# Kernel tuning notes

Hardware: AMD Instinct MI355X
Metric: run time of the kernel (lower is better)

The kernel has to match this reference:

```python
import jax, jax.numpy as jnp
import numpy as np

N = 20000       # nodes
E = 320000      # edges (before self-loops)
F_IN = 128
HID = 128
HEADS = 4
OUT_DIM = 2
B = 64          # graphs in batch
SLOPE = 0.2     # GATv2 leaky_relu negative slope (PyG default)


def _glorot(key, shape):
    fan_in, fan_out = shape[0], shape[1]
    limit = np.sqrt(6.0 / (fan_in + fan_out)).astype(np.float32)
    return jax.random.uniform(key, shape, jnp.float32, -limit, limit)


def setup_inputs() -> dict:
    key = jax.random.key(0)
    ks = jax.random.split(key, 24)
    inp = {
        'x': jax.random.normal(ks[0], (N, F_IN), jnp.float32),
        'edge_src': jax.random.randint(ks[1], (E,), 0, N),
        'edge_dst': jax.random.randint(ks[2], (E,), 0, N),
        'batch': jnp.sort(jax.random.randint(ks[3], (N,), 0, B)),
        # layer 1: in=F_IN, out=HEADS*HID, concat
        'Wl1': _glorot(ks[4], (F_IN, HEADS * HID)),
        'Wr1': _glorot(ks[5], (F_IN, HEADS * HID)),
        'bl1': jnp.zeros((HEADS * HID,), jnp.float32),
        'br1': jnp.zeros((HEADS * HID,), jnp.float32),
        'att1': _glorot(ks[6], (HEADS, HID)),
        'bias1': jnp.zeros((HEADS * HID,), jnp.float32),
        # layer 2: in=HEADS*HID, out=HEADS*HID, concat
        'Wl2': _glorot(ks[7], (HEADS * HID, HEADS * HID)),
        'Wr2': _glorot(ks[8], (HEADS * HID, HEADS * HID)),
        'bl2': jnp.zeros((HEADS * HID,), jnp.float32),
        'br2': jnp.zeros((HEADS * HID,), jnp.float32),
        'att2': _glorot(ks[9], (HEADS, HID)),
        'bias2': jnp.zeros((HEADS * HID,), jnp.float32),
        # layer 3: in=HEADS*HID, heads=1, concat=False -> out=HID
        'Wl3': _glorot(ks[10], (HEADS * HID, HID)),
        'Wr3': _glorot(ks[11], (HEADS * HID, HID)),
        'bl3': jnp.zeros((HID,), jnp.float32),
        'br3': jnp.zeros((HID,), jnp.float32),
        'att3': _glorot(ks[12], (1, HID)),
        'bias3': jnp.zeros((HID,), jnp.float32),
        # output MLP
        'W_mlp1': _glorot(ks[13], (HID, HID)),
        'b_mlp1': jnp.zeros((HID,), jnp.float32),
        'W_mlp2': _glorot(ks[14], (HID, OUT_DIM)),
        'b_mlp2': jnp.zeros((OUT_DIM,), jnp.float32),
    }
    return inp


def gatv2_layer(x, src, dst, Wl, Wr, bl, br, att, bias, concat):
    """PyG GATv2Conv (eval mode): alpha_ij = softmax_j over N(i) of a^T LeakyReLU(xl_j + xr_i)."""
    H, C = att.shape
    n = x.shape[0]
    xl = (x @ Wl + bl).reshape(n, H, C)   # source transform
    e = jax.nn.leaky_relu(xl[src] + (x @ Wr + br).reshape(n, H, C)[dst], SLOPE)  # [E,H,C]
    logits = jnp.einsum('ehc,hc->eh', e, att)                                    # [E,H]
    # segment softmax over destination node
    m = jax.ops.segment_max(logits, dst, num_segments=n)
    alpha = jnp.exp(logits - m[dst])
    denom = jax.ops.segment_sum(alpha, dst, num_segments=n)
    alpha = alpha / denom[dst]
    out = jax.ops.segment_sum(xl[src] * alpha[..., None], dst, num_segments=n)   # [N,H,C]
    out = out.reshape(n, H * C) if concat else out.mean(axis=1)
    return out + bias


def reference(x, edge_src, edge_dst, batch,
              Wl1, Wr1, bl1, br1, att1, bias1,
              Wl2, Wr2, bl2, br2, att2, bias2,
              Wl3, Wr3, bl3, br3, att3, bias3,
              W_mlp1, b_mlp1, W_mlp2, b_mlp2):
    n = x.shape[0]
    loop = jnp.arange(n, dtype=edge_src.dtype)
    src = jnp.concatenate([edge_src, loop])   # PyG add_self_loops=True
    dst = jnp.concatenate([edge_dst, loop])

    h = jax.nn.elu(gatv2_layer(x, src, dst, Wl1, Wr1, bl1, br1, att1, bias1, True))
    h = jax.nn.elu(gatv2_layer(h, src, dst, Wl2, Wr2, bl2, br2, att2, bias2, True))
    h = jax.nn.elu(gatv2_layer(h, src, dst, Wl3, Wr3, bl3, br3, att3, bias3, False))

    # global_mean_pool over graph ids
    counts = jnp.maximum(jax.ops.segment_sum(jnp.ones((n,), h.dtype), batch, num_segments=B), 1.0)
    pooled = jax.ops.segment_sum(h, batch, num_segments=B) / counts[:, None]

    hidden = jax.nn.relu(pooled @ W_mlp1 + b_mlp1)
    return hidden @ W_mlp2 + b_mlp2
```

## Files before the change

kernel.cpp:

```cpp
#include <hip/hip_runtime.h>
#include <math.h>


typedef __attribute__((ext_vector_type(4))) float f32x4;
typedef __attribute__((ext_vector_type(8))) _Float16 f16x8;
typedef __attribute__((ext_vector_type(4))) _Float16 f16x4;
typedef __attribute__((ext_vector_type(2))) _Float16 f16x2;

__device__ __forceinline__ float elu1(float x) {
    return (x > 0.f) ? x : (__expf(x) - 1.f);
}
__device__ __forceinline__ float leaky02(float x) {
    return (x >= 0.f) ? x : 0.2f * x;
}
__device__ __forceinline__ f16x2 pk_leaky(f16x2 s) {
    const f16x2 slope = {(_Float16)0.2f, (_Float16)0.2f};
    return __builtin_elementwise_max(s, s * slope);
}

__global__ void zero32_kernel(int* __restrict__ p, int n) {
    int i = blockIdx.x * 256 + threadIdx.x;
    if (i < n) p[i] = 0;
}

__global__ void count_kernel(const int* __restrict__ dst, int* __restrict__ cnt,
                             int E, int N) {
    int e = blockIdx.x * 256 + threadIdx.x;
    if (e < E + N) {
        int d = (e < E) ? dst[e] : (e - E);
        atomicAdd(&cnt[d], 1);
    }
}

__global__ __launch_bounds__(1024) void scan_kernel(const int* __restrict__ cnt,
                                                    int* __restrict__ rowstart,
                                                    int* __restrict__ cursor,
                                                    int N, int total) {
    __shared__ int part[1024];
    int t = threadIdx.x;
    int ch = (N + 1023) >> 10;
    int base = t * ch;
    int loc[32];
    int s = 0;
    for (int i = 0; i < ch && i < 32; ++i) {
        int idx = base + i;
        int v = (idx < N) ? cnt[idx] : 0;
        loc[i] = s;
        s += v;
    }
    part[t] = s;
    __syncthreads();
    for (int off = 1; off < 1024; off <<= 1) {
        int v = (t >= off) ? part[t - off] : 0;
        __syncthreads();
        part[t] += v;
        __syncthreads();
    }
    int excl = (t == 0) ? 0 : part[t - 1];
    for (int i = 0; i < ch && i < 32; ++i) {
        int idx = base + i;
        if (idx < N) {
            int v = excl + loc[i];
            rowstart[idx] = v;
            cursor[idx]   = v;
        }
    }
    if (t == 0) rowstart[N] = total;
}

__global__ void scatter_kernel(const int* __restrict__ src, const int* __restrict__ dst,
                               int* __restrict__ cursor, int* __restrict__ csr_src,
                               int E, int N) {
    int e = blockIdx.x * 256 + threadIdx.x;
    if (e < E + N) {
        int d, s;
        if (e < E) { d = dst[e]; s = src[e]; }
        else       { d = e - E; s = e - E; }
        int pos = atomicAdd(&cursor[d], 1);
        csr_src[pos] = s;
    }
}

__global__ void boundary_kernel(const int* __restrict__ batch,
                                int* __restrict__ gstart, int N, int B) {
    int n = blockIdx.x * 256 + threadIdx.x;
    if (n > N) return;
    int cur  = (n < N) ? batch[n] : B;
    int prev = (n == 0) ? -1 : batch[n - 1];
    for (int g = prev + 1; g <= cur; ++g) gstart[g] = n;
}

__global__ void convA_kernel(const float* __restrict__ X, _Float16* __restrict__ A,
                             int n_valid, int n_total) {
    int i = (blockIdx.x * 256 + threadIdx.x) * 4;
    if (i >= n_total) return;
    float4 v = (i < n_valid) ? *(const float4*)(X + i) : make_float4(0.f, 0.f, 0.f, 0.f);
    f16x4 h;
    h.x = (_Float16)v.x; h.y = (_Float16)v.y;
    h.z = (_Float16)v.z; h.w = (_Float16)v.w;
    *(f16x4*)(A + i) = h;
}

__global__ __launch_bounds__(256) void convWT_kernel(
    const float* __restrict__ Wl, const float* __restrict__ Wr,
    _Float16* __restrict__ Bth, _Float16* __restrict__ Btl, int K, int Nh) {
    __shared__ float tile[32][33];
    int kb = blockIdx.x * 32;
    int nb = blockIdx.y * 32;
    int tx = threadIdx.x;
    int ty = threadIdx.y;
#pragma unroll
    for (int j = 0; j < 4; ++j) {
        int kk = kb + ty + j * 8;
        int nn = nb + tx;
        float v = (nn < Nh) ? Wl[(size_t)kk * Nh + nn]
                            : Wr[(size_t)kk * Nh + (nn - Nh)];
        tile[ty + j * 8][tx] = v;
    }
    __syncthreads();
#pragma unroll
    for (int j = 0; j < 4; ++j) {
        int nn = nb + ty + j * 8;
        int kk = kb + tx;
        float v = tile[tx][ty + j * 8];
        _Float16 h = (_Float16)v;
        Bth[(size_t)nn * K + kk] = h;
        Btl[(size_t)nn * K + kk] = (_Float16)(v - (float)h);
    }
}

#define SCW 132
__global__ __launch_bounds__(256, 1) void gemm_f16_kernel(
    const _Float16* __restrict__ A,
    const _Float16* __restrict__ Bh, const _Float16* __restrict__ Bl,
    const float* __restrict__ biasL, const float* __restrict__ biasR, int Nh_,
    _Float16* __restrict__ P, _Float16* __restrict__ Q, int K, int NT) {
    __shared__ __align__(16) char smem[49152];
    _Float16* sA[2]  = { (_Float16*)(smem),         (_Float16*)(smem + 24576) };
    _Float16* sBh[2] = { (_Float16*)(smem + 8192),  (_Float16*)(smem + 32768) };
    _Float16* sBl[2] = { (_Float16*)(smem + 16384), (_Float16*)(smem + 40960) };
    float*    sC     = (float*)(smem);

    const int tid  = threadIdx.x;
    const int lane = tid & 63;
    const int wv   = tid >> 6;
    const int wm   = wv & 1;
    const int wn   = wv >> 1;
    const int fm   = lane & 15;
    const int q    = lane >> 4;

    const int bi = blockIdx.x;
    const int kx = bi & 7;
    const int tt = bi >> 3;
    const int m0 = ((tt / NT) * 8 + kx) * 128;
    const int n0 = (tt % NT) * 128;

    const int r0  = lane >> 2;
    const int kco = (lane & 3) << 3;

    f32x4 acc[4][4];
#pragma unroll
    for (int i = 0; i < 4; ++i)
#pragma unroll
        for (int j = 0; j < 4; ++j) {
            acc[i][j].x = 0.f; acc[i][j].y = 0.f;
            acc[i][j].z = 0.f; acc[i][j].w = 0.f;
        }

    for (int k0 = 0; k0 < K; k0 += 64) {
        __syncthreads();
#pragma unroll
        for (int s = 0; s < 2; ++s) {
            int ks = k0 + s * 32;
#pragma unroll
            for (int j = 0; j < 2; ++j) {
                int wc  = wv * 2 + j;
                int row = wc * 16 + r0;
                size_t ga = (size_t)(m0 + row) * K + ks + kco;
                size_t gb = (size_t)(n0 + row) * K + ks + kco;
                int lofs = wc * 512;
                __builtin_amdgcn_global_load_lds(
                    (const __attribute__((address_space(1))) void*)(A + ga),
                    (__attribute__((address_space(3))) void*)(sA[s] + lofs), 16, 0, 0);
                __builtin_amdgcn_global_load_lds(
                    (const __attribute__((address_space(1))) void*)(Bh + gb),
                    (__attribute__((address_space(3))) void*)(sBh[s] + lofs), 16, 0, 0);
                __builtin_amdgcn_global_load_lds(
                    (const __attribute__((address_space(1))) void*)(Bl + gb),
                    (__attribute__((address_space(3))) void*)(sBl[s] + lofs), 16, 0, 0);
            }
        }
        __syncthreads();

#pragma unroll
        for (int s = 0; s < 2; ++s) {
            f16x8 ah[4];
#pragma unroll
            for (int mi = 0; mi < 4; ++mi)
                ah[mi] = *(const f16x8*)&sA[s][(wm * 64 + mi * 16 + fm) * 32 + q * 8];
#pragma unroll
            for (int ni = 0; ni < 4; ++ni) {
                int r = (wn * 64 + ni * 16 + fm) * 32 + q * 8;
                f16x8 bh = *(const f16x8*)&sBh[s][r];
                f16x8 bl = *(const f16x8*)&sBl[s][r];
#pragma unroll
                for (int mi = 0; mi < 4; ++mi) {
                    acc[mi][ni] = __builtin_amdgcn_mfma_f32_16x16x32_f16(ah[mi], bh, acc[mi][ni], 0, 0, 0);
                    acc[mi][ni] = __builtin_amdgcn_mfma_f32_16x16x32_f16(ah[mi], bl, acc[mi][ni], 0, 0, 0);
                }
            }
        }
    }

    float bsv[4];
#pragma unroll
    for (int ni = 0; ni < 4; ++ni) {
        int col = n0 + wn * 64 + ni * 16 + fm;
        bsv[ni] = (col < Nh_) ? biasL[col] : biasR[col - Nh_];
    }

    _Float16* dstbase = (n0 < Nh_) ? P : Q;
    const int col0 = (n0 < Nh_) ? n0 : (n0 - Nh_);

#pragma unroll
    for (int c = 0; c < 2; ++c) {
        __syncthreads();
        if (wm == c) {
#pragma unroll
            for (int mi = 0; mi < 4; ++mi)
#pragma unroll
                for (int ni = 0; ni < 4; ++ni) {
                    int base = (mi * 16 + q * 4) * SCW + wn * 64 + ni * 16 + fm;
                    sC[base]           = acc[mi][ni].x + bsv[ni];
                    sC[base + SCW]     = acc[mi][ni].y + bsv[ni];
                    sC[base + 2 * SCW] = acc[mi][ni].z + bsv[ni];
                    sC[base + 3 * SCW] = acc[mi][ni].w + bsv[ni];
                }
        }
        __syncthreads();
#pragma unroll
        for (int j = 0; j < 8; ++j) {
            int flat = j * 256 + tid;
            int row  = flat >> 5;
            int col  = (flat & 31) * 4;
            f32x4 v = *(const f32x4*)(sC + row * SCW + col);
            f16x4 hv;
            hv.x = (_Float16)v.x; hv.y = (_Float16)v.y;
            hv.z = (_Float16)v.z; hv.w = (_Float16)v.w;
            *(f16x4*)(dstbase + (size_t)(m0 + c * 64 + row) * Nh_ + col0 + col) = hv;
        }
    }
}

__global__ __launch_bounds__(256) void gat_edge4_kernel(
    const _Float16* __restrict__ P, const _Float16* __restrict__ Q,
    const float* __restrict__ att, const float* __restrict__ bias,
    const int* __restrict__ rowstart, const int* __restrict__ srcs,
    _Float16* __restrict__ H, int N) {
    __shared__ float s_m[4][4];
    __shared__ float s_l[4][4];
    __shared__ float s_acc[4][512];

    int n = blockIdx.x;
    int wv = threadIdx.x >> 6;
    int lane = threadIdx.x & 63;
    int c0 = lane * 8;
    int h = lane >> 4;

    f16x8 rv = *(const f16x8*)(Q + (size_t)n * 512 + c0);
    f16x2 r2[4];
#pragma unroll
    for (int k = 0; k < 4; ++k) { r2[k].x = rv[2 * k]; r2[k].y = rv[2 * k + 1]; }
    float tf[8];
#pragma unroll
    for (int j = 0; j < 8; ++j) tf[j] = att[c0 + j];

    float acc[8];
#pragma unroll
    for (int j = 0; j < 8; ++j) acc[j] = 0.f;
    float m_run = -1e30f, l_run = 0.f;

    int beg = rowstart[n], end = rowstart[n + 1];
    int i = beg + wv * 2;
    for (; i + 1 < end; i += 8) {
        int s0 = srcs[i];
        int s1 = srcs[i + 1];
        f16x8 hv0 = *(const f16x8*)(P + (size_t)s0 * 512 + c0);
        f16x8 hv1 = *(const f16x8*)(P + (size_t)s1 * 512 + c0);
        float p0 = 0.f, p1 = 0.f;
#pragma unroll
        for (int k = 0; k < 4; ++k) {
            f16x2 a0; a0.x = hv0[2 * k]; a0.y = hv0[2 * k + 1];
            f16x2 a1; a1.x = hv1[2 * k]; a1.y = hv1[2 * k + 1];
            f16x2 m0v = pk_leaky(a0 + r2[k]);
            f16x2 m1v = pk_leaky(a1 + r2[k]);
            p0 = fmaf((float)m0v.x, tf[2 * k], p0);
            p0 = fmaf((float)m0v.y, tf[2 * k + 1], p0);
            p1 = fmaf((float)m1v.x, tf[2 * k], p1);
            p1 = fmaf((float)m1v.y, tf[2 * k + 1], p1);
        }
        p0 += __shfl_xor(p0, 1, 16);
        p1 += __shfl_xor(p1, 1, 16);
        p0 += __shfl_xor(p0, 2, 16);
        p1 += __shfl_xor(p1, 2, 16);
        p0 += __shfl_xor(p0, 4, 16);
        p1 += __shfl_xor(p1, 4, 16);
        p0 += __shfl_xor(p0, 8, 16);
        p1 += __shfl_xor(p1, 8, 16);
        float m01 = fmaxf(p0, p1);
        float w0 = __expf(p0 - m01);
        float w1 = __expf(p1 - m01);
        float pl = w0 + w1;
        float m_new = fmaxf(m_run, m01);
        float sc = __expf(m_run - m_new);
        float sp = __expf(m01 - m_new);
        l_run = l_run * sc + pl * sp;
        float ws0 = w0 * sp;
        float ws1 = w1 * sp;
#pragma unroll
        for (int j = 0; j < 8; ++j) {
            float a = acc[j] * sc;
            a = fmaf((float)hv0[j], ws0, a);
            acc[j] = fmaf((float)hv1[j], ws1, a);
        }
        m_run = m_new;
    }
    if (i < end) {
        int s = srcs[i];
        f16x8 hv = *(const f16x8*)(P + (size_t)s * 512 + c0);
        float p = 0.f;
#pragma unroll
        for (int k = 0; k < 4; ++k) {
            f16x2 a; a.x = hv[2 * k]; a.y = hv[2 * k + 1];
            f16x2 mv = pk_leaky(a + r2[k]);
            p = fmaf((float)mv.x, tf[2 * k], p);
            p = fmaf((float)mv.y, tf[2 * k + 1], p);
        }
        p += __shfl_xor(p, 1, 16);
        p += __shfl_xor(p, 2, 16);
        p += __shfl_xor(p, 4, 16);
        p += __shfl_xor(p, 8, 16);
        float m_new = fmaxf(m_run, p);
        float sc = __expf(m_run - m_new);
        float al = __expf(p - m_new);
        l_run = l_run * sc + al;
#pragma unroll
        for (int j = 0; j < 8; ++j)
            acc[j] = fmaf((float)hv[j], al, acc[j] * sc);
        m_run = m_new;
    }
    if ((lane & 15) == 0) { s_m[wv][h] = m_run; s_l[wv][h] = l_run; }
    *(float4*)&s_acc[wv][c0]     = make_float4(acc[0], acc[1], acc[2], acc[3]);
    *(float4*)&s_acc[wv][c0 + 4] = make_float4(acc[4], acc[5], acc[6], acc[7]);
    __syncthreads();
    if (wv == 0) {
        float M = fmaxf(fmaxf(s_m[0][h], s_m[1][h]), fmaxf(s_m[2][h], s_m[3][h]));
        float L = 0.f;
        float o[8];
#pragma unroll
        for (int j = 0; j < 8; ++j) o[j] = 0.f;
#pragma unroll
        for (int w = 0; w < 4; ++w) {
            float sc = __expf(s_m[w][h] - M);
            L += s_l[w][h] * sc;
            float4 q0 = *(const float4*)&s_acc[w][c0];
            float4 q1 = *(const float4*)&s_acc[w][c0 + 4];
            o[0] += q0.x * sc; o[1] += q0.y * sc; o[2] += q0.z * sc; o[3] += q0.w * sc;
            o[4] += q1.x * sc; o[5] += q1.y * sc; o[6] += q1.z * sc; o[7] += q1.w * sc;
        }
        float inv = 1.f / L;
        f16x8 oh;
#pragma unroll
        for (int j = 0; j < 8; ++j)
            oh[j] = (_Float16)elu1(o[j] * inv + bias[c0 + j]);
        *(f16x8*)(H + (size_t)n * 512 + c0) = oh;
    }
}

__global__ __launch_bounds__(256) void gat_edge1_kernel(
    const _Float16* __restrict__ P, const _Float16* __restrict__ Q,
    const float* __restrict__ att, const float* __restrict__ bias,
    const int* __restrict__ rowstart, const int* __restrict__ srcs,
    float* __restrict__ out, int N) {
    __shared__ float s_m[4];
    __shared__ float s_l[4];
    __shared__ float s_acc[4][128];

    int n = blockIdx.x;
    int wv = threadIdx.x >> 6;
    int lane = threadIdx.x & 63;
    int c0 = lane * 2;

    f16x2 rv = *(const f16x2*)(Q + (size_t)n * 128 + c0);
    float2 t = *(const float2*)(att + c0);

    float acc0 = 0.f, acc1 = 0.f;
    float m_run = -1e30f, l_run = 0.f;

    int beg = rowstart[n], end = rowstart[n + 1];
    int i = beg + wv * 2;
    for (; i + 1 < end; i += 8) {
        int s0 = srcs[i];
        int s1 = srcs[i + 1];
        f16x2 h0 = *(const f16x2*)(P + (size_t)s0 * 128 + c0);
        f16x2 h1 = *(const f16x2*)(P + (size_t)s1 * 128 + c0);
        f16x2 m0v = pk_leaky(h0 + rv);
        f16x2 m1v = pk_leaky(h1 + rv);
        float p0 = fmaf((float)m0v.x, t.x, (float)m0v.y * t.y);
        float p1 = fmaf((float)m1v.x, t.x, (float)m1v.y * t.y);
        p0 += __shfl_xor(p0, 1, 64);
        p1 += __shfl_xor(p1, 1, 64);
        p0 += __shfl_xor(p0, 2, 64);
        p1 += __shfl_xor(p1, 2, 64);
        p0 += __shfl_xor(p0, 4, 64);
        p1 += __shfl_xor(p1, 4, 64);
        p0 += __shfl_xor(p0, 8, 64);
        p1 += __shfl_xor(p1, 8, 64);
        p0 += __shfl_xor(p0, 16, 64);
        p1 += __shfl_xor(p1, 16, 64);
        p0 += __shfl_xor(p0, 32, 64);
        p1 += __shfl_xor(p1, 32, 64);
        float m01 = fmaxf(p0, p1);
        float w0 = __expf(p0 - m01);
        float w1 = __expf(p1 - m01);
        float pl  = w0 + w1;
        float m_new = fmaxf(m_run, m01);
        float sc = __expf(m_run - m_new);
        float sp = __expf(m01 - m_new);
        float ws0 = w0 * sp;
        float ws1 = w1 * sp;
        l_run = l_run * sc + pl * sp;
        acc0 = fmaf((float)h1.x, ws1, fmaf((float)h0.x, ws0, acc0 * sc));
        acc1 = fmaf((float)h1.y, ws1, fmaf((float)h0.y, ws0, acc1 * sc));
        m_run = m_new;
    }
    if (i < end) {
        int s = srcs[i];
        f16x2 hv = *(const f16x2*)(P + (size_t)s * 128 + c0);
        f16x2 mv = pk_leaky(hv + rv);
        float p = fmaf((float)mv.x, t.x, (float)mv.y * t.y);
        p += __shfl_xor(p, 1, 64);
        p += __shfl_xor(p, 2, 64);
        p += __shfl_xor(p, 4, 64);
        p += __shfl_xor(p, 8, 64);
        p += __shfl_xor(p, 16, 64);
        p += __shfl_xor(p, 32, 64);
        float m_new = fmaxf(m_run, p);
        float sc = __expf(m_run - m_new);
        float al = __expf(p - m_new);
        l_run = l_run * sc + al;
        acc0 = fmaf((float)hv.x, al, acc0 * sc);
        acc1 = fmaf((float)hv.y, al, acc1 * sc);
        m_run = m_new;
    }
    if (lane == 0) { s_m[wv] = m_run; s_l[wv] = l_run; }
    *(float2*)&s_acc[wv][c0] = make_float2(acc0, acc1);
    __syncthreads();
    if (wv == 0) {
        float M = fmaxf(fmaxf(s_m[0], s_m[1]), fmaxf(s_m[2], s_m[3]));
        float L = 0.f, o0 = 0.f, o1 = 0.f;
#pragma unroll
        for (int w = 0; w < 4; ++w) {
            float sc = __expf(s_m[w] - M);
            L += s_l[w] * sc;
            float2 qv = *(const float2*)&s_acc[w][c0];
            o0 += qv.x * sc;
            o1 += qv.y * sc;
        }
        float inv = 1.f / L;
        float2 w2;
        w2.x = elu1(o0 * inv + bias[c0]);
        w2.y = elu1(o1 * inv + bias[c0 + 1]);
        *(float2*)(out + (size_t)n * 128 + c0) = w2;
    }
}

__global__ __launch_bounds__(256) void pool2_kernel(
    const float* __restrict__ h3, const int* __restrict__ gstart,
    float* __restrict__ pooled) {
    __shared__ float red[256];
    int g = blockIdx.x;
    int c = threadIdx.x & 127;
    int h = threadIdx.x >> 7;
    int gs = gstart[g], ge = gstart[g + 1];
    float s = 0.f;
    for (int n = gs + h; n < ge; n += 2) s += h3[(size_t)n * 128 + c];
    red[threadIdx.x] = s;
    __syncthreads();
    if (h == 0) {
        float tot = red[c] + red[c + 128];
        float cnt = fmaxf((float)(ge - gs), 1.f);
        pooled[g * 128 + c] = tot / cnt;
    }
}

__global__ __launch_bounds__(128) void mlp_kernel(
    const float* __restrict__ pooled,
    const float* __restrict__ W1, const float* __restrict__ b1,
    const float* __restrict__ W2, const float* __restrict__ b2,
    float* __restrict__ out) {
    __shared__ float pr[128];
    __shared__ float2 red[128];
    int g = blockIdx.x;
    int t = threadIdx.x;
    pr[t] = pooled[g * 128 + t];
    __syncthreads();
    float h = b1[t];
#pragma unroll 4
    for (int k = 0; k < 128; ++k) h = fmaf(pr[k], W1[k * 128 + t], h);
    h = fmaxf(h, 0.0f);
    red[t] = make_float2(h * W2[t * 2], h * W2[t * 2 + 1]);
    __syncthreads();
    for (int s = 64; s > 0; s >>= 1) {
        if (t < s) {
            red[t].x += red[t + s].x;
            red[t].y += red[t + s].y;
        }
        __syncthreads();
    }
    if (t == 0) {
        out[g * 2]     = red[0].x + b2[0];
        out[g * 2 + 1] = red[0].y + b2[1];
    }
}

extern "C" void kernel_launch(void* const* d_in, const int* in_sizes, int n_in,
                              void* d_out, int out_size, void* d_ws, size_t ws_size,
                              hipStream_t stream) {
    const float* x     = (const float*)d_in[0];
    const int*   esrc  = (const int*)d_in[1];
    const int*   edst  = (const int*)d_in[2];
    const int*   batch = (const int*)d_in[3];
    const float* Wl1   = (const float*)d_in[4];
    const float* Wr1   = (const float*)d_in[5];
    const float* bl1   = (const float*)d_in[6];
    const float* br1   = (const float*)d_in[7];
    const float* att1  = (const float*)d_in[8];
    const float* bias1 = (const float*)d_in[9];
    const float* Wl2   = (const float*)d_in[10];
    const float* Wr2   = (const float*)d_in[11];
    const float* bl2   = (const float*)d_in[12];
    const float* br2   = (const float*)d_in[13];
    const float* att2  = (const float*)d_in[14];
    const float* bias2 = (const float*)d_in[15];
    const float* Wl3   = (const float*)d_in[16];
    const float* Wr3   = (const float*)d_in[17];
    const float* bl3   = (const float*)d_in[18];
    const float* br3   = (const float*)d_in[19];
    const float* att3  = (const float*)d_in[20];
    const float* bias3 = (const float*)d_in[21];
    const float* Wm1   = (const float*)d_in[22];
    const float* bm1   = (const float*)d_in[23];
    const float* Wm2   = (const float*)d_in[24];
    const float* bm2   = (const float*)d_in[25];

    int N  = in_sizes[0] / 128;
    int E  = in_sizes[1];
    int ET = E + N;
    int B  = out_size / 2;
    const int Mp = 160 * 128;

    char* ws = (char*)d_ws;
    size_t off = 0;
    auto alloc = [&](size_t bytes) -> void* {
        void* p = ws + off;
        off += (bytes + 255) & ~(size_t)255;
        return p;
    };
    _Float16* P    = (_Float16*)alloc((size_t)Mp * 512 * 2);
    _Float16* Q    = (_Float16*)alloc((size_t)Mp * 512 * 2);
    _Float16* A1   = (_Float16*)alloc((size_t)Mp * 128 * 2);
    _Float16* Hb   = (_Float16*)alloc((size_t)Mp * 512 * 2);
    _Float16* Wth1 = (_Float16*)alloc((size_t)1024 * 128 * 2);
    _Float16* Wtl1 = (_Float16*)alloc((size_t)1024 * 128 * 2);
    _Float16* Wth2 = (_Float16*)alloc((size_t)1024 * 512 * 2);
    _Float16* Wtl2 = (_Float16*)alloc((size_t)1024 * 512 * 2);
    _Float16* Wth3 = (_Float16*)alloc((size_t)256 * 512 * 2);
    _Float16* Wtl3 = (_Float16*)alloc((size_t)256 * 512 * 2);
    float*    R3   = (float*)alloc((size_t)Mp * 128 * 4);
    int*    cnt      = (int*)alloc((size_t)N * 4);
    int*    rowstart = (int*)alloc((size_t)(N + 1) * 4);
    int*    cursor   = (int*)alloc((size_t)N * 4);
    int*    csr_src  = (int*)alloc((size_t)ET * 4);
    int*    gstart   = (int*)alloc((size_t)(B + 1) * 4);
    float*  pooled   = (float*)alloc((size_t)B * 128 * 4);
    (void)ws_size;

    zero32_kernel<<<(N + 255) / 256, 256, 0, stream>>>(cnt, N);

    count_kernel<<<(ET + 255) / 256, 256, 0, stream>>>(edst, cnt, E, N);
    scan_kernel<<<1, 1024, 0, stream>>>(cnt, rowstart, cursor, N, ET);
    scatter_kernel<<<(ET + 255) / 256, 256, 0, stream>>>(esrc, edst, cursor, csr_src, E, N);
    boundary_kernel<<<(N + 256) / 256, 256, 0, stream>>>(batch, gstart, N, B);

    convWT_kernel<<<dim3(4, 32),  dim3(32, 8), 0, stream>>>(Wl1, Wr1, Wth1, Wtl1, 128, 512);
    convWT_kernel<<<dim3(16, 32), dim3(32, 8), 0, stream>>>(Wl2, Wr2, Wth2, Wtl2, 512, 512);
    convWT_kernel<<<dim3(16, 8),  dim3(32, 8), 0, stream>>>(Wl3, Wr3, Wth3, Wtl3, 512, 128);

    convA_kernel<<<((Mp * 128 / 4) + 255) / 256, 256, 0, stream>>>(x, A1, N * 128, Mp * 128);

    gemm_f16_kernel<<<160 * 8, 256, 0, stream>>>(A1, Wth1, Wtl1, bl1, br1, 512, P, Q, 128, 8);
    gat_edge4_kernel<<<N, 256, 0, stream>>>(P, Q, att1, bias1, rowstart, csr_src, Hb, N);

    gemm_f16_kernel<<<160 * 8, 256, 0, stream>>>(Hb, Wth2, Wtl2, bl2, br2, 512, P, Q, 512, 8);
    gat_edge4_kernel<<<N, 256, 0, stream>>>(P, Q, att2, bias2, rowstart, csr_src, Hb, N);

    gemm_f16_kernel<<<160 * 2, 256, 0, stream>>>(Hb, Wth3, Wtl3, bl3, br3, 128, P, Q, 512, 2);
    gat_edge1_kernel<<<N, 256, 0, stream>>>(P, Q, att3, bias3, rowstart, csr_src, R3, N);

    pool2_kernel<<<B, 256, 0, stream>>>(R3, gstart, pooled);
    mlp_kernel<<<B, 128, 0, stream>>>(pooled, Wm1, bm1, Wm2, bm2, (float*)d_out);
}
```

Baseline: 469.7 us.

## Double-buffer GEMM K-loop to prefetch the next slice during MFMA

```diff
diff --git a/kernel.cpp b/kernel.cpp
--- a/kernel.cpp
+++ b/kernel.cpp
@@ -9,9 +9,6 @@
 
 __device__ __forceinline__ float elu1(float x) {
     return (x > 0.f) ? x : (__expf(x) - 1.f);
-}
-__device__ __forceinline__ float leaky02(float x) {
-    return (x >= 0.f) ? x : 0.2f * x;
 }
 __device__ __forceinline__ f16x2 pk_leaky(f16x2 s) {
     const f16x2 slope = {(_Float16)0.2f, (_Float16)0.2f};
@@ -136,10 +133,7 @@
     const float* __restrict__ biasL, const float* __restrict__ biasR, int Nh_,
     _Float16* __restrict__ P, _Float16* __restrict__ Q, int K, int NT) {
     __shared__ __align__(16) char smem[49152];
-    _Float16* sA[2]  = { (_Float16*)(smem),         (_Float16*)(smem + 24576) };
-    _Float16* sBh[2] = { (_Float16*)(smem + 8192),  (_Float16*)(smem + 32768) };
-    _Float16* sBl[2] = { (_Float16*)(smem + 16384), (_Float16*)(smem + 40960) };
-    float*    sC     = (float*)(smem);
+    float* sC = (float*)(smem);
 
     const int tid  = threadIdx.x;
     const int lane = tid & 63;
@@ -158,6 +152,7 @@
     const int r0  = lane >> 2;
     const int kco = (lane & 3) << 3;
 
+
     f32x4 acc[4][4];
 #pragma unroll
     for (int i = 0; i < 4; ++i)
@@ -167,49 +162,71 @@
             acc[i][j].z = 0.f; acc[i][j].w = 0.f;
         }
 
-    for (int k0 = 0; k0 < K; k0 += 64) {
+    const int nIters = K >> 5;
+    int cur = 0;
+    {
+        char* base = smem;
+#pragma unroll
+        for (int j = 0; j < 2; ++j) {
+            int wc  = wv * 2 + j;
+            int row = wc * 16 + r0;
+            size_t ga = (size_t)(m0 + row) * K + kco;
+            size_t gb = (size_t)(n0 + row) * K + kco;
+            int lofs = wc * 1024;
+            __builtin_amdgcn_global_load_lds(
+                (const __attribute__((address_space(1))) void*)(A + ga),
+                (__attribute__((address_space(3))) void*)(base + lofs), 16, 0, 0);
+            __builtin_amdgcn_global_load_lds(
+                (const __attribute__((address_space(1))) void*)(Bh + gb),
+                (__attribute__((address_space(3))) void*)(base + 8192 + lofs), 16, 0, 0);
+            __builtin_amdgcn_global_load_lds(
+                (const __attribute__((address_space(1))) void*)(Bl + gb),
+                (__attribute__((address_space(3))) void*)(base + 16384 + lofs), 16, 0, 0);
+        }
+    }
+    for (int it = 0; it < nIters; ++it) {
         __syncthreads();
-#pragma unroll
-        for (int s = 0; s < 2; ++s) {
-            int ks = k0 + s * 32;
+        if (it + 1 < nIters) {
+            char* base = smem + (cur ^ 1) * 24576;
+            int ks = (it + 1) << 5;
 #pragma unroll
             for (int j = 0; j < 2; ++j) {
                 int wc  = wv * 2 + j;
                 int row = wc * 16 + r0;
                 size_t ga = (size_t)(m0 + row) * K + ks + kco;
                 size_t gb = (size_t)(n0 + row) * K + ks + kco;
-                int lofs = wc * 512;
+                int lofs = wc * 1024;
                 __builtin_amdgcn_global_load_lds(
                     (const __attribute__((address_space(1))) void*)(A + ga),
-                    (__attribute__((address_space(3))) void*)(sA[s] + lofs), 16, 0, 0);
+                    (__attribute__((address_space(3))) void*)(base + lofs), 16, 0, 0);
                 __builtin_amdgcn_global_load_lds(
                     (const __attribute__((address_space(1))) void*)(Bh + gb),
-                    (__attribute__((address_space(3))) void*)(sBh[s] + lofs), 16, 0, 0);
+                    (__attribute__((address_space(3))) void*)(base + 8192 + lofs), 16, 0, 0);
                 __builtin_amdgcn_global_load_lds(
                     (const __attribute__((address_space(1))) void*)(Bl + gb),
-                    (__attribute__((address_space(3))) void*)(sBl[s] + lofs), 16, 0, 0);
+                    (__attribute__((address_space(3))) void*)(base + 16384 + lofs), 16, 0, 0);
             }
         }
-        __syncthreads();
-
-#pragma unroll
-        for (int s = 0; s < 2; ++s) {
-            f16x8 ah[4];
-#pragma unroll
-            for (int mi = 0; mi < 4; ++mi)
-                ah[mi] = *(const f16x8*)&sA[s][(wm * 64 + mi * 16 + fm) * 32 + q * 8];
-#pragma unroll
-            for (int ni = 0; ni < 4; ++ni) {
-                int r = (wn * 64 + ni * 16 + fm) * 32 + q * 8;
-                f16x8 bh = *(const f16x8*)&sBh[s][r];
-                f16x8 bl = *(const f16x8*)&sBl[s][r];
-#pragma unroll
-                for (int mi = 0; mi < 4; ++mi) {
-                    acc[mi][ni] = __builtin_amdgcn_mfma_f32_16x16x32_f16(ah[mi], bh, acc[mi][ni], 0, 0, 0);
-                    acc[mi][ni] = __builtin_amdgcn_mfma_f32_16x16x32_f16(ah[mi], bl, acc[mi][ni], 0, 0, 0);
-                }
+
+        _Float16* cA  = (_Float16*)(smem + cur * 24576);
+        _Float16* cBh = (_Float16*)(smem + cur * 24576 + 8192);
+        _Float16* cBl = (_Float16*)(smem + cur * 24576 + 16384);
+        f16x8 ah[4];
+#pragma unroll
+        for (int mi = 0; mi < 4; ++mi)
+            ah[mi] = *(const f16x8*)&cA[(wm * 64 + mi * 16 + fm) * 32 + q * 8];
+#pragma unroll
+        for (int ni = 0; ni < 4; ++ni) {
+            int r = (wn * 64 + ni * 16 + fm) * 32 + q * 8;
+            f16x8 bh = *(const f16x8*)&cBh[r];
+            f16x8 bl = *(const f16x8*)&cBl[r];
+#pragma unroll
+            for (int mi = 0; mi < 4; ++mi) {
+                acc[mi][ni] = __builtin_amdgcn_mfma_f32_16x16x32_f16(ah[mi], bh, acc[mi][ni], 0, 0, 0);
+                acc[mi][ni] = __builtin_amdgcn_mfma_f32_16x16x32_f16(ah[mi], bl, acc[mi][ni], 0, 0, 0);
             }
         }
+        cur ^= 1;
     }
 
     float bsv[4];
```

New measurement: 448.4 us. 4.5% less time.
